# Kernel tuning notes

Hardware: AMD Instinct MI355X
Metric: run time of the kernel (lower is better)

The kernel has to match this reference:

```python
import jax, jax.numpy as jnp
import numpy as np

LN_EPS = 1e-5
TOP_K = 2


def setup_inputs() -> dict:
    key = jax.random.key(0)
    ks = jax.random.split(key, 6)
    B, S, D, I, E = 4, 1024, 1024, 4096, 8
    return {
        "hidden_states": jax.random.normal(ks[0], (B, S, D), dtype=jnp.float32),
        "attention_mask": jnp.ones((B, S), dtype=jnp.float32),
        "gate_w": jax.random.normal(ks[1], (E, D), dtype=jnp.float32) * 0.02,
        "w1": jax.random.normal(ks[2], (E, D, I), dtype=jnp.float32) * 0.02,
        "b1": jnp.zeros((E, I), dtype=jnp.float32),
        "w2": jax.random.normal(ks[3], (E, I, D), dtype=jnp.float32) * 0.02,
        "b2": jnp.zeros((E, D), dtype=jnp.float32),
        "ln_gamma": jnp.ones((D,), dtype=jnp.float32),
        "ln_beta": jnp.zeros((D,), dtype=jnp.float32),
    }


def reference(hidden_states, attention_mask, gate_w, w1, b1, w2, b2, ln_gamma, ln_beta):
    B, S, D = hidden_states.shape
    E = gate_w.shape[0]
    h = hidden_states.reshape(-1, D).astype(jnp.float32)  # (T, D)

    # --- gate: softmax over experts, top-2, renormalize ---
    logits = h @ gate_w.T                                  # (T, E)
    probs = jax.nn.softmax(logits, axis=-1)
    rw, sel = jax.lax.top_k(probs, TOP_K)                  # (T, k), (T, k)
    rw = rw / jnp.sum(rw, axis=-1, keepdims=True)

    # per-token dense combine weights: (T, E), zero for non-selected experts
    onehot = jax.nn.one_hot(sel, E, dtype=rw.dtype)        # (T, k, E)
    w_te = jnp.einsum('tk,tke->te', rw, onehot)            # (T, E)

    # --- expert FFNs (dense over all experts; weights zero-out non-selected) ---
    mid = jax.nn.gelu(jnp.einsum('td,edi->eti', h, w1) + b1[:, None, :], approximate=False)
    eout = jnp.einsum('eti,eid->etd', mid, w2) + b2[:, None, :]  # (E, T, D)
    moe_out = jnp.einsum('etd,te->td', eout, w_te)         # (T, D)

    out = moe_out.reshape(B, S, D) * attention_mask[..., None]
    out = hidden_states + out

    # LayerNorm
    mu = jnp.mean(out, axis=-1, keepdims=True)
    var = jnp.var(out, axis=-1, keepdims=True)
    out = (out - mu) * jax.lax.rsqrt(var + LN_EPS) * ln_gamma + ln_beta

    # load balancing loss: mse(expert_usage, uniform)
    T = h.shape[0]
    usage = jnp.sum(onehot, axis=(0, 1)) / T               # (E,)
    aux_loss = jnp.mean((usage - 1.0 / E) ** 2)
    return out, aux_loss
```

## Files before the change

### kernel.cpp

```cpp
#include <hip/hip_runtime.h>
#include <hip/hip_bf16.h>
#include <math.h>

#define T_TOK 4096
#define D_DIM 1024
#define I_DIM 4096
#define E_EXP 8
#define MAX_TILES 72

typedef __attribute__((ext_vector_type(8))) short bf16x8;
typedef __attribute__((ext_vector_type(4))) float f32x4;

__device__ __forceinline__ unsigned short f2bf(float x) {
    unsigned int u = __float_as_uint(x);
    u += 0x7fffu + ((u >> 16) & 1u);
    return (unsigned short)(u >> 16);
}

__device__ __forceinline__ void glds16(const unsigned short* g, unsigned short* l) {
    __builtin_amdgcn_global_load_lds(
        (const __attribute__((address_space(1))) unsigned int*)g,
        (__attribute__((address_space(3))) unsigned int*)(unsigned int)(unsigned long long)(void*)l,
        16, 0, 0);
}

#define VMWAIT4 asm volatile("s_waitcnt vmcnt(4)" ::: "memory")
#define VMWAIT0 asm volatile("s_waitcnt vmcnt(0)" ::: "memory")

__device__ __forceinline__ void bar() {
    asm volatile("" ::: "memory");
    __builtin_amdgcn_s_barrier();
    asm volatile("" ::: "memory");
}

__global__ void gate_kernel(const float* __restrict__ h, const float* __restrict__ gw,
                            int* __restrict__ counts, int* __restrict__ sel,
                            float* __restrict__ wgt, unsigned short* __restrict__ Hbf) {
    int t = blockIdx.x;
    int tid = threadIdx.x;
    const int d4 = tid * 4;
    const float4 hv = *(const float4*)(h + (size_t)t * D_DIM + d4);
    union { unsigned short u[4]; ushort4 v; } o;
    o.u[0] = f2bf(hv.x); o.u[1] = f2bf(hv.y); o.u[2] = f2bf(hv.z); o.u[3] = f2bf(hv.w);
    *(ushort4*)(Hbf + (size_t)t * D_DIM + d4) = o.v;

    float acc[E_EXP];
#pragma unroll
    for (int e = 0; e < E_EXP; e++) {
        const float4 g = *(const float4*)(gw + e * D_DIM + d4);
        acc[e] = hv.x * g.x + hv.y * g.y + hv.z * g.z + hv.w * g.w;
    }
#pragma unroll
    for (int e = 0; e < E_EXP; e++)
        for (int off = 32; off > 0; off >>= 1) acc[e] += __shfl_down(acc[e], off, 64);
    __shared__ float red[4][E_EXP];
    int wave = tid >> 6, lane = tid & 63;
    if (lane == 0) {
#pragma unroll
        for (int e = 0; e < E_EXP; e++) red[wave][e] = acc[e];
    }
    __syncthreads();
    if (tid == 0) {
        float lg[E_EXP];
#pragma unroll
        for (int e = 0; e < E_EXP; e++) lg[e] = red[0][e] + red[1][e] + red[2][e] + red[3][e];
        float mx = lg[0];
#pragma unroll
        for (int e = 1; e < E_EXP; e++) mx = fmaxf(mx, lg[e]);
        float p[E_EXP];
#pragma unroll
        for (int e = 0; e < E_EXP; e++) p[e] = expf(lg[e] - mx);
        int i0 = 0; float b0 = p[0];
#pragma unroll
        for (int e = 1; e < E_EXP; e++) if (p[e] > b0) { b0 = p[e]; i0 = e; }
        int i1 = -1; float b1v = -1.f;
#pragma unroll
        for (int e = 0; e < E_EXP; e++) if (e != i0 && p[e] > b1v) { b1v = p[e]; i1 = e; }
        float den = b0 + b1v;
        sel[2 * t] = i0; sel[2 * t + 1] = i1;
        wgt[2 * t] = b0 / den; wgt[2 * t + 1] = b1v / den;
        atomicAdd(&counts[i0], 1);
        atomicAdd(&counts[i1], 1);
    }
}

__global__ void offsets_kernel(const int* __restrict__ counts, int* __restrict__ offs,
                               int* __restrict__ cursors, float* __restrict__ aux_out,
                               int* __restrict__ tile_e, int* __restrict__ tile_m,
                               int* __restrict__ ntiles) {
    if (blockIdx.x == 0 && threadIdx.x == 0) {
        int off = 0; float aux = 0.f; int nt = 0;
        for (int e = 0; e < E_EXP; e++) {
            offs[e] = off; off += counts[e]; cursors[e] = 0;
            float u = (float)counts[e] / (float)T_TOK;
            float d = u - 1.0f / (float)E_EXP;
            aux += d * d;
            for (int m0 = 0; m0 < counts[e]; m0 += 128) {
                tile_e[nt] = e; tile_m[nt] = m0; nt++;
            }
        }
        ntiles[0] = nt;
        aux_out[0] = aux / (float)E_EXP;
    }
}

__global__ void scatter_kernel(const int* __restrict__ sel, const float* __restrict__ wgt,
                               const int* __restrict__ offs, int* __restrict__ cursors,
                               int* __restrict__ tok_list, float* __restrict__ tok_w,
                               int* __restrict__ slot_of) {
    int t = blockIdx.x * 256 + threadIdx.x;
    if (t >= T_TOK) return;
#pragma unroll
    for (int k = 0; k < 2; k++) {
        int e = sel[2 * t + k];
        int pos = atomicAdd(&cursors[e], 1);
        int idx = offs[e] + pos;
        tok_list[idx] = t;
        tok_w[idx] = wgt[2 * t + k];
        slot_of[2 * t + k] = idx;
    }
}

__global__ void transpose_cvt2_kernel(const float* __restrict__ w1, const float* __restrict__ w2,
                                      unsigned short* __restrict__ W1t, unsigned short* __restrict__ W2t) {
    __shared__ float tile[64][65];
    const int z = blockIdx.y;
    const bool isW1 = (z < 8);
    const int e = isW1 ? z : z - 8;
    const int R = isW1 ? D_DIM : I_DIM;
    const int C = isW1 ? I_DIM : D_DIM;
    const float* s = (isW1 ? w1 : w2) + (size_t)e * R * C;
    unsigned short* d = (isW1 ? W1t : W2t) + (size_t)e * R * C;
    const int tpc = C >> 6;
    const int tr = blockIdx.x / tpc, tc = blockIdx.x % tpc;
    const int r0 = tr * 64, c0 = tc * 64;
    const int tid = threadIdx.x;
    const int rr = tid >> 4;
    const int c4 = (tid & 15) * 4;
#pragma unroll
    for (int p = 0; p < 4; p++) {
        const float4 v = *(const float4*)(s + (size_t)(r0 + rr + 16 * p) * C + c0 + c4);
        tile[rr + 16 * p][c4]     = v.x;
        tile[rr + 16 * p][c4 + 1] = v.y;
        tile[rr + 16 * p][c4 + 2] = v.z;
        tile[rr + 16 * p][c4 + 3] = v.w;
    }
    __syncthreads();
#pragma unroll
    for (int p = 0; p < 4; p++) {
        const int oc = rr + 16 * p;
        union { unsigned short u[4]; ushort4 v; } o;
#pragma unroll
        for (int k2 = 0; k2 < 4; k2++) o.u[k2] = f2bf(tile[c4 + k2][oc]);
        *(ushort4*)(d + (size_t)(c0 + oc) * R + r0 + c4) = o.v;
    }
}

template <int MODE>
__launch_bounds__(256, 4)
__global__ void moe_gemm_kernel(const unsigned short* __restrict__ Abase,
                                const unsigned short* __restrict__ Bt,
                                const float* __restrict__ bias,
                                const int* __restrict__ counts, const int* __restrict__ offs,
                                const int* __restrict__ tile_e, const int* __restrict__ tile_m,
                                const int* __restrict__ ntiles,
                                const int* __restrict__ tok_list, const float* __restrict__ tok_w,
                                unsigned short* __restrict__ midout, float* __restrict__ slotbuf) {
    constexpr int K  = (MODE == 0) ? D_DIM : I_DIM;
    constexpr int N  = (MODE == 0) ? I_DIM : D_DIM;
    constexpr int NT = K / 32;

    __shared__ __align__(16) unsigned short lA[2][128 * 32];
    __shared__ __align__(16) unsigned short lB[2][128 * 32];

    const int nwg  = gridDim.x * gridDim.y;
    const int flat = blockIdx.y * gridDim.x + blockIdx.x;
    const int q8 = nwg >> 3, r8 = nwg & 7;
    const int xcd = flat & 7, pos = flat >> 3;
    const int id2 = (xcd < r8 ? xcd * (q8 + 1) : r8 * (q8 + 1) + (xcd - r8) * q8) + pos;
    const int tix = id2 / gridDim.y;
    const int nb  = id2 % gridDim.y;
    if (tix >= ntiles[0]) return;

    const int e   = tile_e[tix];
    const int m0  = tile_m[tix];
    const int Ne  = counts[e];
    const int seg = offs[e];
    const int n0  = nb * 128;

    const int tid  = threadIdx.x;
    const int w    = tid >> 6;
    const int lane = tid & 63;
    const int quad = lane >> 4;
    const int l15  = lane & 15;
    const int wm   = (w >> 1) * 64;
    const int wn   = (w & 1) * 64;

    const int lrow = lane >> 2;
    const int scol = (((lane & 3) ^ ((lane >> 3) & 3)) & 3) * 8;
    const int rs   = (((quad ^ ((l15 >> 1) & 3)) & 3) * 8);

    const unsigned short *gA0, *gA1;
    {
        int mr0 = m0 + w * 32 + lrow;
        int mr1 = mr0 + 16;
        int c0 = (mr0 < Ne) ? mr0 : 0;
        int c1 = (mr1 < Ne) ? mr1 : 0;
        size_t r0, r1;
        if (MODE == 0) { r0 = (size_t)tok_list[seg + c0] * K; r1 = (size_t)tok_list[seg + c1] * K; }
        else           { r0 = (size_t)(seg + c0) * K;         r1 = (size_t)(seg + c1) * K; }
        gA0 = Abase + r0 + scol;
        gA1 = Abase + r1 + scol;
    }
    const unsigned short* Bte = Bt + (size_t)e * N * K;
    const unsigned short* gB0 = Bte + (size_t)(n0 + w * 32 + lrow) * K + scol;
    const unsigned short* gB1 = gB0 + (size_t)16 * K;

    auto STAGE = [&](int t) {
        const int b = t & 1, off = t * 32;
        glds16(gA0 + off, &lA[b][(w * 32) * 32]);
        glds16(gA1 + off, &lA[b][(w * 32 + 16) * 32]);
        glds16(gB0 + off, &lB[b][(w * 32) * 32]);
        glds16(gB1 + off, &lB[b][(w * 32 + 16) * 32]);
    };

    f32x4 acc[4][4];
#pragma unroll
    for (int i = 0; i < 4; i++)
#pragma unroll
        for (int j = 0; j < 4; j++) acc[i][j] = (f32x4){0.f, 0.f, 0.f, 0.f};

    STAGE(0);
    for (int kt = 0; kt < NT; ++kt) {
        if (kt + 1 < NT) {
            STAGE(kt + 1);
            VMWAIT4;
        } else {
            VMWAIT0;
        }
        bar();
        const unsigned short* LA = lA[kt & 1];
        const unsigned short* LB = lB[kt & 1];
        bf16x8 av[4], bv[4];
#pragma unroll
        for (int i = 0; i < 4; i++)
            av[i] = *(const bf16x8*)&LA[(wm + i * 16 + l15) * 32 + rs];
#pragma unroll
        for (int j = 0; j < 4; j++)
            bv[j] = *(const bf16x8*)&LB[(wn + j * 16 + l15) * 32 + rs];
        __builtin_amdgcn_s_setprio(1);
#pragma unroll
        for (int i = 0; i < 4; i++)
#pragma unroll
            for (int j = 0; j < 4; j++)
                acc[i][j] = __builtin_amdgcn_mfma_f32_16x16x32_bf16(av[i], bv[j], acc[i][j], 0, 0, 0);
        __builtin_amdgcn_s_setprio(0);
        bar();
    }

    const float* be = bias + (size_t)e * N;
#pragma unroll
    for (int i = 0; i < 4; i++) {
        const int mbase = m0 + wm + i * 16 + quad * 4;
#pragma unroll
        for (int j = 0; j < 4; j++) {
            const int n = n0 + wn + j * 16 + l15;
            const float bvl = be[n];
#pragma unroll
            for (int r = 0; r < 4; r++) {
                const int m = mbase + r;
                if (m < Ne) {
                    float v = acc[i][j][r] + bvl;
                    if (MODE == 0) {
                        v = 0.5f * v * (1.0f + erff(v * 0.70710678118654752f));
                        midout[(size_t)(seg + m) * N + n] = f2bf(v);
                    } else {
                        slotbuf[(size_t)(seg + m) * N + n] = tok_w[seg + m] * v;
                    }
                }
            }
        }
    }
}

__global__ void ln_kernel(const float* __restrict__ hs, const float* __restrict__ mask,
                          const float* __restrict__ slotbuf, const int* __restrict__ slot_of,
                          const float* __restrict__ gamma, const float* __restrict__ beta,
                          float* __restrict__ outp) {
    int t = blockIdx.x, tid = threadIdx.x;
    int s0 = slot_of[2 * t], s1 = slot_of[2 * t + 1];
    float mk = mask[t];
    const float4* hr = (const float4*)(hs + (size_t)t * D_DIM);
    const float4* p0 = (const float4*)(slotbuf + (size_t)s0 * D_DIM);
    const float4* p1 = (const float4*)(slotbuf + (size_t)s1 * D_DIM);
    float4 hv = hr[tid], a = p0[tid], b = p1[tid];
    float x0 = hv.x + mk * (a.x + b.x);
    float x1 = hv.y + mk * (a.y + b.y);
    float x2 = hv.z + mk * (a.z + b.z);
    float x3 = hv.w + mk * (a.w + b.w);
    float sum = x0 + x1 + x2 + x3;
    float sq = x0 * x0 + x1 * x1 + x2 * x2 + x3 * x3;
    for (int off = 32; off > 0; off >>= 1) {
        sum += __shfl_down(sum, off, 64);
        sq += __shfl_down(sq, off, 64);
    }
    __shared__ float rsum[4], rsq[4];
    __shared__ float mu_s, rstd_s;
    int wave = tid >> 6, lane = tid & 63;
    if (lane == 0) { rsum[wave] = sum; rsq[wave] = sq; }
    __syncthreads();
    if (tid == 0) {
        float s = rsum[0] + rsum[1] + rsum[2] + rsum[3];
        float q = rsq[0] + rsq[1] + rsq[2] + rsq[3];
        float mu = s / (float)D_DIM;
        float var = q / (float)D_DIM - mu * mu;
        mu_s = mu; rstd_s = rsqrtf(var + 1e-5f);
    }
    __syncthreads();
    float mu = mu_s, rstd = rstd_s;
    const float4* g4 = (const float4*)gamma;
    const float4* b4 = (const float4*)beta;
    float4 g = g4[tid], bb = b4[tid];
    float4 o;
    o.x = (x0 - mu) * rstd * g.x + bb.x;
    o.y = (x1 - mu) * rstd * g.y + bb.y;
    o.z = (x2 - mu) * rstd * g.z + bb.z;
    o.w = (x3 - mu) * rstd * g.w + bb.w;
    ((float4*)(outp + (size_t)t * D_DIM))[tid] = o;
}

extern "C" void kernel_launch(void* const* d_in, const int* in_sizes, int n_in,
                              void* d_out, int out_size, void* d_ws, size_t ws_size,
                              hipStream_t stream) {
    const float* hs    = (const float*)d_in[0];
    const float* mask  = (const float*)d_in[1];
    const float* gw    = (const float*)d_in[2];
    const float* w1    = (const float*)d_in[3];
    const float* b1    = (const float*)d_in[4];
    const float* w2    = (const float*)d_in[5];
    const float* b2    = (const float*)d_in[6];
    const float* gamma = (const float*)d_in[7];
    const float* beta  = (const float*)d_in[8];
    float* out = (float*)d_out;

    char* ws = (char*)d_ws;
    int*   counts   = (int*)(ws + 0);
    int*   cursors  = (int*)(ws + 64);
    int*   offs     = (int*)(ws + 128);
    int*   ntiles   = (int*)(ws + 256);
    int*   tile_e   = (int*)(ws + 512);
    int*   tile_m   = (int*)(ws + 1024);
    int*   sel      = (int*)(ws + 4096);
    float* wgt      = (float*)(ws + 4096 + 1 * 32768);
    int*   slot_of  = (int*)(ws + 4096 + 2 * 32768);
    int*   tok_list = (int*)(ws + 4096 + 3 * 32768);
    float* tok_w    = (float*)(ws + 4096 + 4 * 32768);
    unsigned short* Hbf = (unsigned short*)(ws + (1ull << 20));
    unsigned short* W1t = (unsigned short*)(ws + (9ull << 20));
    unsigned short* W2t = (unsigned short*)(ws + (73ull << 20));
    unsigned short* mid = (unsigned short*)(ws + (137ull << 20));
    float* slotbuf      = (float*)(ws + (201ull << 20));

    hipMemsetAsync(counts, 0, 64, stream);
    gate_kernel<<<T_TOK, 256, 0, stream>>>(hs, gw, counts, sel, wgt, Hbf);
    offsets_kernel<<<1, 64, 0, stream>>>(counts, offs, cursors, out + (size_t)T_TOK * D_DIM,
                                         tile_e, tile_m, ntiles);
    scatter_kernel<<<T_TOK / 256, 256, 0, stream>>>(sel, wgt, offs, cursors, tok_list, tok_w, slot_of);
    transpose_cvt2_kernel<<<dim3(1024, 16), 256, 0, stream>>>(w1, w2, W1t, W2t);
    moe_gemm_kernel<0><<<dim3(MAX_TILES, I_DIM / 128), 256, 0, stream>>>(
        Hbf, W1t, b1, counts, offs, tile_e, tile_m, ntiles, tok_list, tok_w, mid, nullptr);
    moe_gemm_kernel<1><<<dim3(MAX_TILES, D_DIM / 128), 256, 0, stream>>>(
        mid, W2t, b2, counts, offs, tile_e, tile_m, ntiles, tok_list, tok_w, nullptr, slotbuf);
    ln_kernel<<<T_TOK, 256, 0, stream>>>(hs, mask, slotbuf, slot_of, gamma, beta, out);
}
```

Baseline: 723.1 us.

## Load A fragments directly from global into registers, keep only B in LDS

Drops the LDS staging buffer for the A operand. Each lane now loads its MFMA A fragments straight from global memory into registers, prefetched two k-steps ahead with double-buffered register sets, while B stays on the global_load_lds double buffer. The main loop is unrolled by two and the wait counts are adjusted to match. Launch bounds drop to 2 waves per SIMD to leave room for the extra registers. This cuts LDS traffic and shared-memory footprint, but it gives up A reuse across the two waves that share rows, so global/L2 traffic for A roughly doubles, occupancy may drop, and the vmcnt accounting becomes fragile.

```diff
diff --git a/kernel.cpp b/kernel.cpp
--- a/kernel.cpp
+++ b/kernel.cpp
@@ -24,7 +24,7 @@
         16, 0, 0);
 }
 
-#define VMWAIT4 asm volatile("s_waitcnt vmcnt(4)" ::: "memory")
+#define VMWAIT6 asm volatile("s_waitcnt vmcnt(6)" ::: "memory")
 #define VMWAIT0 asm volatile("s_waitcnt vmcnt(0)" ::: "memory")
 
 __device__ __forceinline__ void bar() {
@@ -157,7 +157,7 @@
 }
 
 template <int MODE>
-__launch_bounds__(256, 4)
+__launch_bounds__(256, 2)
 __global__ void moe_gemm_kernel(const unsigned short* __restrict__ Abase,
                                 const unsigned short* __restrict__ Bt,
                                 const float* __restrict__ bias,
@@ -170,7 +170,6 @@
     constexpr int N  = (MODE == 0) ? I_DIM : D_DIM;
     constexpr int NT = K / 32;
 
-    __shared__ __align__(16) unsigned short lA[2][128 * 32];
     __shared__ __align__(16) unsigned short lB[2][128 * 32];
 
     const int nwg  = gridDim.x * gridDim.y;
@@ -200,29 +199,32 @@
     const int scol = (((lane & 3) ^ ((lane >> 3) & 3)) & 3) * 8;
     const int rs   = (((quad ^ ((l15 >> 1) & 3)) & 3) * 8);
 
-    const unsigned short *gA0, *gA1;
-    {
-        int mr0 = m0 + w * 32 + lrow;
-        int mr1 = mr0 + 16;
-        int c0 = (mr0 < Ne) ? mr0 : 0;
-        int c1 = (mr1 < Ne) ? mr1 : 0;
-        size_t r0, r1;
-        if (MODE == 0) { r0 = (size_t)tok_list[seg + c0] * K; r1 = (size_t)tok_list[seg + c1] * K; }
-        else           { r0 = (size_t)(seg + c0) * K;         r1 = (size_t)(seg + c1) * K; }
-        gA0 = Abase + r0 + scol;
-        gA1 = Abase + r1 + scol;
-    }
+    const unsigned short* gAr[4];
+#pragma unroll
+    for (int i = 0; i < 4; i++) {
+        int mrow = m0 + wm + i * 16 + l15;
+        int crow = (mrow < Ne) ? mrow : 0;
+        size_t rbase;
+        if (MODE == 0) rbase = (size_t)tok_list[seg + crow] * K;
+        else           rbase = (size_t)(seg + crow) * K;
+        gAr[i] = Abase + rbase + quad * 8;
+    }
+
     const unsigned short* Bte = Bt + (size_t)e * N * K;
     const unsigned short* gB0 = Bte + (size_t)(n0 + w * 32 + lrow) * K + scol;
     const unsigned short* gB1 = gB0 + (size_t)16 * K;
 
-    auto STAGE = [&](int t) {
-        const int b = t & 1, off = t * 32;
-        glds16(gA0 + off, &lA[b][(w * 32) * 32]);
-        glds16(gA1 + off, &lA[b][(w * 32 + 16) * 32]);
+    auto STAGE_B = [&](int t) {
+        const int b = t & 1;
+        const int off = t * 32;
         glds16(gB0 + off, &lB[b][(w * 32) * 32]);
         glds16(gB1 + off, &lB[b][(w * 32 + 16) * 32]);
     };
+    auto LOADA = [&](int t, bf16x8* dst) {
+#pragma unroll
+        for (int i = 0; i < 4; i++)
+            dst[i] = *(const bf16x8*)(gAr[i] + (size_t)t * 32);
+    };
 
     f32x4 acc[4][4];
 #pragma unroll
@@ -230,31 +232,43 @@
 #pragma unroll
         for (int j = 0; j < 4; j++) acc[i][j] = (f32x4){0.f, 0.f, 0.f, 0.f};
 
-    STAGE(0);
-    for (int kt = 0; kt < NT; ++kt) {
-        if (kt + 1 < NT) {
-            STAGE(kt + 1);
-            VMWAIT4;
+    bf16x8 avA[4], avB[4];
+
+    auto COMPUTE = [&](int t, const bf16x8* av) {
+        const unsigned short* LB = lB[t & 1];
+        bf16x8 bv[4];
+#pragma unroll
+        for (int j = 0; j < 4; j++)
+            bv[j] = *(const bf16x8*)&LB[(wn + j * 16 + l15) * 32 + rs];
+        __builtin_amdgcn_s_setprio(1);
+#pragma unroll
+        for (int i = 0; i < 4; i++)
+#pragma unroll
+            for (int j = 0; j < 4; j++)
+                acc[i][j] = __builtin_amdgcn_mfma_f32_16x16x32_bf16(av[i], bv[j], acc[i][j], 0, 0, 0);
+        __builtin_amdgcn_s_setprio(0);
+    };
+
+    STAGE_B(0);
+    LOADA(0, avA);
+    LOADA(1, avB);
+
+    for (int kt = 0; kt < NT; kt += 2) {
+        STAGE_B(kt + 1);
+        VMWAIT6;
+        bar();
+        COMPUTE(kt, avA);
+        if (kt + 2 < NT) LOADA(kt + 2, avA);
+        bar();
+        if (kt + 2 < NT) {
+            STAGE_B(kt + 2);
+            VMWAIT6;
         } else {
             VMWAIT0;
         }
         bar();
-        const unsigned short* LA = lA[kt & 1];
-        const unsigned short* LB = lB[kt & 1];
-        bf16x8 av[4], bv[4];
-#pragma unroll
-        for (int i = 0; i < 4; i++)
-            av[i] = *(const bf16x8*)&LA[(wm + i * 16 + l15) * 32 + rs];
-#pragma unroll
-        for (int j = 0; j < 4; j++)
-            bv[j] = *(const bf16x8*)&LB[(wn + j * 16 + l15) * 32 + rs];
-        __builtin_amdgcn_s_setprio(1);
-#pragma unroll
-        for (int i = 0; i < 4; i++)
-#pragma unroll
-            for (int j = 0; j < 4; j++)
-                acc[i][j] = __builtin_amdgcn_mfma_f32_16x16x32_bf16(av[i], bv[j], acc[i][j], 0, 0, 0);
-        __builtin_amdgcn_s_setprio(0);
+        COMPUTE(kt + 1, avB);
+        if (kt + 3 < NT) LOADA(kt + 3, avB);
         bar();
     }
 
```

New measurement: 892.8 us. +23.5%, slower.
